# Performance work log

Measured on AMD Instinct MI355X. Metric: run time of the kernel, lower is better.

## Reference

```python
import jax, jax.numpy as jnp
import numpy as np

EMBED_DIM = 512
NUM_TYPES = 26
PER_TYPE = 128
NUM_CODES = NUM_TYPES * PER_TYPE
COMMIT = 0.25
TEMP = 0.07
N_TOKENS = 32768
SAMPLED_PER_TYPE = int(0.1 * PER_TYPE)  # 12


def _normalize(v, axis=-1):
    # matches F.normalize(p=2) with eps clamp
    return v / jnp.clip(jnp.linalg.norm(v, axis=axis, keepdims=True), 1e-12)


def setup_inputs() -> dict:
    key = jax.random.key(0)
    k1, k2, k3, k4 = jax.random.split(key, 4)
    x = jax.random.normal(k1, (N_TOKENS, EMBED_DIM), jnp.float32)
    Q = jax.random.randint(k2, (N_TOKENS,), 0, NUM_TYPES)
    initrange = 1.0 / EMBED_DIM
    emb = jax.random.uniform(k3, (NUM_CODES, EMBED_DIM), jnp.float32, -initrange, initrange)
    emb = _normalize(emb)  # mirrors _initialize_embeddings
    # deterministic stand-in for torch.randperm(num_per_type)[:sampled_num]
    perm = jax.random.permutation(k4, PER_TYPE)[:SAMPLED_PER_TYPE]
    sampled_indices = (jnp.arange(NUM_TYPES)[:, None] * PER_TYPE + perm[None, :]).reshape(-1)
    return {"x": x, "embeddings": emb, "Q": Q, "sampled_indices": sampled_indices}


def _code_indices(xn, embeddings, Q):
    # full [N, num_codes] squared distances, then select the 128-code slab of
    # each token's PTM type and argmin within it (equivalent to the per-type loop)
    d = ((xn ** 2).sum(-1, keepdims=True)
         + (embeddings ** 2).sum(-1)[None, :]
         - 2.0 * (xn @ embeddings.T))                      # [N, NUM_CODES]
    d = d.reshape(xn.shape[0], NUM_TYPES, PER_TYPE)
    d_sel = jnp.take_along_axis(d, Q[:, None, None], axis=1)[:, 0, :]  # [N, PER_TYPE]
    return jnp.argmin(d_sel, axis=1) + Q * PER_TYPE


def _uniform_loss(embeddings, sampled_indices):
    ne = _normalize(embeddings)
    se = ne[sampled_indices]                               # [S, D]
    sim = se @ se.T                                        # [S, S]
    labels = sampled_indices // PER_TYPE
    pos = (labels[None, :] == labels[:, None]).astype(jnp.float32)
    S = sampled_indices.shape[0]
    eye = jnp.eye(S, dtype=bool)
    sim = jnp.where(eye, -jnp.inf, sim)
    sim_exp = jnp.exp(sim / TEMP)                          # exp(-inf) = 0 kills diagonal
    sum_exp = sim_exp.sum(axis=1)
    pos_sum = (sim_exp * pos).sum(axis=1)
    return -jnp.log(pos_sum / sum_exp).mean()


def reference(x, embeddings, Q, sampled_indices):
    xn = _normalize(x)
    idx = _code_indices(xn, embeddings, Q)
    quantized = _normalize(embeddings[idx])
    q_latent = jnp.mean((quantized - jax.lax.stop_gradient(xn)) ** 2)
    e_latent = jnp.mean((xn - jax.lax.stop_gradient(quantized)) ** 2)
    loss = q_latent + COMMIT * e_latent
    uloss = _uniform_loss(embeddings, sampled_indices)
    out = xn + jax.lax.stop_gradient(quantized - xn)       # straight-through
    return out, loss, uloss, idx
```

## Files before the change

### kernel.cpp

```cpp
#include <hip/hip_runtime.h>
#include <math.h>

#define NTOK   32768
#define DIM    512
#define NTYPES 26
#define PT     128
#define NCODES 3328
#define NSAMP  312
#define INV_TEMP (1.0f / 0.07f)
#define MAXTILES 24

typedef __attribute__((ext_vector_type(8))) short short8;
typedef __attribute__((ext_vector_type(4))) float floatx4;

__device__ __forceinline__ void f2bf2(float f, unsigned short& h, unsigned short& l) {
    unsigned u = __float_as_uint(f);
    unsigned hb = (u + 0x7fffu + ((u >> 16) & 1u)) >> 16;
    h = (unsigned short)hb;
    float hf = __uint_as_float(hb << 16);
    float r = f - hf;
    unsigned u2 = __float_as_uint(r);
    l = (unsigned short)((u2 + 0x7fffu + ((u2 >> 16) & 1u)) >> 16);
}

__global__ __launch_bounds__(256) void k_emb(const float* __restrict__ emb,
                                             unsigned short* __restrict__ Bhg,
                                             unsigned short* __restrict__ Blg,
                                             float* __restrict__ sume,
                                             float* __restrict__ rinv,
                                             int* __restrict__ counts,
                                             float* __restrict__ accg) {
    int tid = threadIdx.x;
    if (blockIdx.x == 0) {
        if (tid < NTYPES) counts[tid] = 0;
        if (tid == 32) accg[0] = 0.0f;
        if (tid == 33) accg[1] = 0.0f;
    }
    int wv = tid >> 6, lane = tid & 63;
    int c = blockIdx.x * 4 + wv;
    const float4* row = (const float4*)(emb + (size_t)c * DIM);
    float4 v0 = row[lane * 2], v1 = row[lane * 2 + 1];
    float s = v0.x*v0.x + v0.y*v0.y + v0.z*v0.z + v0.w*v0.w
            + v1.x*v1.x + v1.y*v1.y + v1.z*v1.z + v1.w*v1.w;
    for (int m = 32; m; m >>= 1) s += __shfl_xor(s, m);
    if (lane == 0) {
        sume[c] = s;
        rinv[c] = 1.0f / fmaxf(sqrtf(s), 1e-12f);
    }
    union { short8 v; unsigned short u[8]; } hh, ll;
    f2bf2(v0.x, hh.u[0], ll.u[0]); f2bf2(v0.y, hh.u[1], ll.u[1]);
    f2bf2(v0.z, hh.u[2], ll.u[2]); f2bf2(v0.w, hh.u[3], ll.u[3]);
    f2bf2(v1.x, hh.u[4], ll.u[4]); f2bf2(v1.y, hh.u[5], ll.u[5]);
    f2bf2(v1.z, hh.u[6], ll.u[6]); f2bf2(v1.w, hh.u[7], ll.u[7]);
    *(short8*)(Bhg + (size_t)c * DIM + lane * 8) = hh.v;
    *(short8*)(Blg + (size_t)c * DIM + lane * 8) = ll.v;
}

__global__ __launch_bounds__(256) void k_hist(const int* __restrict__ Q,
                                              int* __restrict__ counts,
                                              int* __restrict__ rank) {
    __shared__ int lbin[NTYPES];
    __shared__ int lbase[NTYPES];
    int tid = threadIdx.x;
    if (tid < NTYPES) lbin[tid] = 0;
    __syncthreads();
    int t = blockIdx.x * 256 + tid;
    int qt = Q[t];
    int lr = atomicAdd(&lbin[qt], 1);
    __syncthreads();
    if (tid < NTYPES) lbase[tid] = atomicAdd(&counts[tid], lbin[tid]);
    __syncthreads();
    rank[t] = lbase[qt] + lr;
}

__global__ __launch_bounds__(256) void k_scatter(const int* __restrict__ Q,
                                                 const int* __restrict__ counts,
                                                 const int* __restrict__ rank,
                                                 int* __restrict__ order,
                                                 int* __restrict__ offsg) {
    __shared__ int offs[NTYPES];
    int tid = threadIdx.x;
    if (tid == 0) {
        int a = 0;
        for (int i = 0; i < NTYPES; i++) {
            offs[i] = a;
            if (blockIdx.x == 0) offsg[i] = a;
            a += counts[i];
        }
        if (blockIdx.x == 0) offsg[NTYPES] = a;
    }
    __syncthreads();
    int t = blockIdx.x * 256 + tid;
    order[offs[Q[t]] + rank[t]] = t;
}

__global__ __launch_bounds__(256, 3) void k_main(const float* __restrict__ x,
                                                 const float* __restrict__ emb,
                                                 const unsigned short* __restrict__ Bhg,
                                                 const unsigned short* __restrict__ Blg,
                                                 const int* __restrict__ order,
                                                 const int* __restrict__ offsg,
                                                 const float* __restrict__ sume,
                                                 const float* __restrict__ rinv,
                                                 float* __restrict__ outbuf,
                                                 float* __restrict__ idxout,
                                                 float* __restrict__ accg) {
    int q = blockIdx.x;
    int tile = blockIdx.y;
    int base = offsg[q];
    int cnt = offsg[q + 1] - base;
    int tstart = tile * 64;
    if (tstart >= cnt) return;
    int nt = min(64, cnt - tstart);

    __shared__ unsigned short Ah[64][72];
    __shared__ unsigned short Al[64][72];
    __shared__ unsigned short Bh[128 * 64];
    __shared__ unsigned short Bl[128 * 64];
    __shared__ int   toks_s[64];
    __shared__ float rn_s[64];
    __shared__ float sume_s[128];
    __shared__ float rinv_s[128];
    __shared__ float redv[64][2];
    __shared__ int   redi[64][2];
    __shared__ int   bestc[64];

    int tid = threadIdx.x;
    int lane = tid & 63;
    int wv = tid >> 6;
    int wm = wv & 1, wn = wv >> 1;
    int lc = lane & 15;
    int q4 = lane >> 4;

    if (tid < 64) toks_s[tid] = order[base + tstart + min(tid, nt - 1)];
    if (tid < 128) {
        sume_s[tid] = sume[q * PT + tid];
        rinv_s[tid] = rinv[q * PT + tid];
    }

    const float* aptr[4];
    int arow = tid >> 4, asg = tid & 15;
#pragma unroll
    for (int i = 0; i < 4; i++) {
        int r = arow + 16 * i;
        int t = order[base + tstart + min(r, nt - 1)];
        aptr[i] = x + (size_t)t * DIM + asg * 4;
    }
    const unsigned short* bh_slab = Bhg + (size_t)q * PT * DIM;
    const unsigned short* bl_slab = Blg + (size_t)q * PT * DIM;
    size_t bofs[4];
#pragma unroll
    for (int i = 0; i < 4; i++) {
        int id = tid + i * 256;
        bofs[i] = (size_t)(id >> 3) * DIM + (id & 7) * 8;
    }

    floatx4 acc[2][4];
#pragma unroll
    for (int mi = 0; mi < 2; mi++)
#pragma unroll
        for (int ni = 0; ni < 4; ni++)
            acc[mi][ni] = (floatx4){0.f, 0.f, 0.f, 0.f};
    float ps[4] = {0.f, 0.f, 0.f, 0.f};

    float4 va[4];
    short8 vbh[4], vbl[4];
#pragma unroll
    for (int i = 0; i < 4; i++) va[i] = *(const float4*)(aptr[i]);
#pragma unroll
    for (int i = 0; i < 4; i++) {
        vbh[i] = *(const short8*)(bh_slab + bofs[i]);
        vbl[i] = *(const short8*)(bl_slab + bofs[i]);
    }

    for (int kc = 0; kc < 8; kc++) {
#pragma unroll
        for (int i = 0; i < 4; i++) {
            int r = arow + 16 * i;
            float4 v = va[i];
            ps[i] = fmaf(v.x, v.x, fmaf(v.y, v.y, fmaf(v.z, v.z, fmaf(v.w, v.w, ps[i]))));
            ushort4 h, l;
            f2bf2(v.x, h.x, l.x); f2bf2(v.y, h.y, l.y);
            f2bf2(v.z, h.z, l.z); f2bf2(v.w, h.w, l.w);
            *(ushort4*)&Ah[r][asg * 4] = h;
            *(ushort4*)&Al[r][asg * 4] = l;
        }
#pragma unroll
        for (int i = 0; i < 4; i++) {
            int id = tid + i * 256;
            int r = id >> 3, p = id & 7;
            int dst = r * 64 + ((p ^ (r & 7)) << 3);
            *(short8*)&Bh[dst] = vbh[i];
            *(short8*)&Bl[dst] = vbl[i];
        }
        __syncthreads();
        if (kc < 7) {
            int k0n = (kc + 1) * 64;
#pragma unroll
            for (int i = 0; i < 4; i++) va[i] = *(const float4*)(aptr[i] + k0n);
#pragma unroll
            for (int i = 0; i < 4; i++) {
                vbh[i] = *(const short8*)(bh_slab + bofs[i] + k0n);
                vbl[i] = *(const short8*)(bl_slab + bofs[i] + k0n);
            }
        }
#pragma unroll
        for (int ks2 = 0; ks2 < 2; ks2++) {
            int ko = ks2 * 32 + q4 * 8;
            int g = ko >> 3;
            short8 ahf[2], alf[2], bhf[4], blf[4];
#pragma unroll
            for (int mi = 0; mi < 2; mi++) {
                int m = wm * 32 + mi * 16 + lc;
                ahf[mi] = *(const short8*)&Ah[m][ko];
                alf[mi] = *(const short8*)&Al[m][ko];
            }
#pragma unroll
            for (int ni = 0; ni < 4; ni++) {
                int n = wn * 64 + ni * 16 + lc;
                int bs = n * 64 + ((g ^ (lc & 7)) << 3);
                bhf[ni] = *(const short8*)&Bh[bs];
                blf[ni] = *(const short8*)&Bl[bs];
            }
#pragma unroll
            for (int mi = 0; mi < 2; mi++)
#pragma unroll
                for (int ni = 0; ni < 4; ni++) {
                    acc[mi][ni] = __builtin_amdgcn_mfma_f32_16x16x32_bf16(ahf[mi], bhf[ni], acc[mi][ni], 0, 0, 0);
                    acc[mi][ni] = __builtin_amdgcn_mfma_f32_16x16x32_bf16(ahf[mi], blf[ni], acc[mi][ni], 0, 0, 0);
                    acc[mi][ni] = __builtin_amdgcn_mfma_f32_16x16x32_bf16(alf[mi], bhf[ni], acc[mi][ni], 0, 0, 0);
                }
        }
        __syncthreads();
    }

#pragma unroll
    for (int m = 1; m <= 8; m <<= 1)
#pragma unroll
        for (int i = 0; i < 4; i++) ps[i] += __shfl_xor(ps[i], m);
    if ((lane & 15) == 0) {
#pragma unroll
        for (int i = 0; i < 4; i++)
            rn_s[arow + 16 * i] = 1.0f / fmaxf(sqrtf(ps[i]), 1e-12f);
    }
    __syncthreads();

#pragma unroll
    for (int mi = 0; mi < 2; mi++) {
#pragma unroll
        for (int r = 0; r < 4; r++) {
            int m = wm * 32 + mi * 16 + q4 * 4 + r;
            float rn2 = -2.0f * rn_s[m];
            float bv = 1e30f; int bc = 0;
#pragma unroll
            for (int ni = 0; ni < 4; ni++) {
                int n = wn * 64 + ni * 16 + lc;
                float d = fmaf(rn2, acc[mi][ni][r], sume_s[n]);
                if (d < bv) { bv = d; bc = n; }
            }
#pragma unroll
            for (int mk = 1; mk <= 8; mk <<= 1) {
                float ov = __shfl_xor(bv, mk);
                int oc = __shfl_xor(bc, mk);
                if (ov < bv || (ov == bv && oc < bc)) { bv = ov; bc = oc; }
            }
            if (lc == 0) { redv[m][wn] = bv; redi[m][wn] = bc; }
        }
    }
    __syncthreads();

    if (tid < 64) {
        float v0 = redv[tid][0], v1 = redv[tid][1];
        int c = (v1 < v0) ? redi[tid][1] : redi[tid][0];
        float bv = fminf(v0, v1);
        bestc[tid] = c;
        float term = 0.0f;
        if (tid < nt) {
            idxout[toks_s[tid]] = (float)(q * PT + c);
            term = 2.0f - (sume_s[c] - bv) * rinv_s[c];
        }
        for (int mk = 32; mk; mk >>= 1) term += __shfl_xor(term, mk);
        if (tid == 0) atomicAdd(&accg[0], term);
    }
    __syncthreads();

    for (int t = wv; t < nt; t += 4) {
        int c = bestc[t];
        int gt = toks_s[t];
        float rv = rinv_s[c];
        const float4* er = (const float4*)(emb + (size_t)(q * PT + c) * DIM);
        float4* orow = (float4*)(outbuf + (size_t)gt * DIM);
#pragma unroll
        for (int s2 = 0; s2 < 2; s2++) {
            float4 ev = er[lane * 2 + s2];
            orow[lane * 2 + s2] = make_float4(ev.x * rv, ev.y * rv, ev.z * rv, ev.w * rv);
        }
    }
}

__global__ __launch_bounds__(256) void k_uloss(const float* __restrict__ emb,
                                               const int* __restrict__ samp,
                                               const float* __restrict__ rinv,
                                               float* __restrict__ accg) {
    __shared__ float rs[4], rp[4];
    int i = blockIdx.x;
    int tid = threadIdx.x;
    int lane = tid & 63, wv = tid >> 6;
    int ci = samp[i];
    float rvi = rinv[ci];
    int labi = ci >> 7;
    const float4* ri = (const float4*)(emb + (size_t)ci * DIM);
    float4 e0 = ri[lane * 2], e1 = ri[lane * 2 + 1];
    float sE = 0.0f, pE = 0.0f;
    for (int j0 = wv; j0 < NSAMP; j0 += 16) {
        float d[4]; int cj[4]; bool val[4];
#pragma unroll
        for (int u = 0; u < 4; u++) {
            int j = j0 + u * 4;
            val[u] = (j < NSAMP) && (j != i);
            int js = val[u] ? j : 0;
            cj[u] = samp[js];
            const float4* rj = (const float4*)(emb + (size_t)cj[u] * DIM);
            float4 f0 = rj[lane * 2], f1 = rj[lane * 2 + 1];
            d[u] = e0.x*f0.x + e0.y*f0.y + e0.z*f0.z + e0.w*f0.w
                 + e1.x*f1.x + e1.y*f1.y + e1.z*f1.z + e1.w*f1.w;
        }
#pragma unroll
        for (int mk = 32; mk; mk >>= 1)
#pragma unroll
            for (int u = 0; u < 4; u++) d[u] += __shfl_xor(d[u], mk);
#pragma unroll
        for (int u = 0; u < 4; u++) {
            float ex = val[u] ? expf(d[u] * rvi * rinv[cj[u]] * INV_TEMP) : 0.0f;
            sE += ex;
            if (val[u] && (cj[u] >> 7) == labi) pE += ex;
        }
    }
    if (lane == 0) { rs[wv] = sE; rp[wv] = pE; }
    __syncthreads();
    if (tid == 0) {
        float S = rs[0] + rs[1] + rs[2] + rs[3];
        float P = rp[0] + rp[1] + rp[2] + rp[3];
        atomicAdd(&accg[1], logf(S) - logf(P));
    }
}

__global__ void k_final(const float* __restrict__ accg, float* __restrict__ lossp) {
    lossp[0] = (1.25f / ((float)NTOK * (float)DIM)) * accg[0];
    lossp[1] = accg[1] / (float)NSAMP;
}

extern "C" void kernel_launch(void* const* d_in, const int* in_sizes, int n_in,
                              void* d_out, int out_size, void* d_ws, size_t ws_size,
                              hipStream_t stream) {
    const float* x   = (const float*)d_in[0];
    const float* emb = (const float*)d_in[1];
    const int* Q     = (const int*)d_in[2];
    const int* samp  = (const int*)d_in[3];

    float* out    = (float*)d_out;
    float* lossp  = out + (size_t)NTOK * DIM;
    float* idxout = out + (size_t)NTOK * DIM + 2;

    unsigned short* Bhg = (unsigned short*)d_ws;
    unsigned short* Blg = Bhg + (size_t)NCODES * DIM;
    float* sume  = (float*)(Blg + (size_t)NCODES * DIM);
    float* rinv  = sume + NCODES;
    int* counts  = (int*)(rinv + NCODES);
    int* offsg   = counts + NTYPES;
    int* rank    = offsg + NTYPES + 1;
    int* order   = rank + NTOK;
    float* accg  = (float*)(order + NTOK);

    k_emb<<<NCODES / 4, 256, 0, stream>>>(emb, Bhg, Blg, sume, rinv, counts, accg);
    k_hist<<<NTOK / 256, 256, 0, stream>>>(Q, counts, rank);
    k_scatter<<<NTOK / 256, 256, 0, stream>>>(Q, counts, rank, order, offsg);
    dim3 gmain(NTYPES, MAXTILES);
    k_main<<<gmain, 256, 0, stream>>>(x, emb, Bhg, Blg, order, offsg, sume, rinv, out, idxout, accg);
    k_uloss<<<NSAMP, 256, 0, stream>>>(emb, samp, rinv, accg);
    k_final<<<1, 1, 0, stream>>>(accg, lossp);
}
```

Baseline: 212.6 us.

## Pre-swizzle codebook into MFMA fragment layout and drop LDS staging in main kernel

The prep kernel now writes the bf16 hi/lo codebook directly in the per-lane MFMA fragment order. Each wave in the main kernel then handles 16 tokens on its own and loads A and B fragments straight from global memory into registers, with no shared-memory tiles or block barriers. Argmin, loss accumulation and output writes are done per wave with shuffles, and launch bounds rise to 4 blocks per CU. This removes LDS traffic and syncs but drops the cross-wave reuse of B, so every wave re-reads the 128-code slab from L2. That raises global/L2 traffic and leaves no software prefetch.

```diff
diff --git a/kernel.cpp b/kernel.cpp
--- a/kernel.cpp
+++ b/kernel.cpp
@@ -52,8 +52,14 @@
     f2bf2(v0.z, hh.u[2], ll.u[2]); f2bf2(v0.w, hh.u[3], ll.u[3]);
     f2bf2(v1.x, hh.u[4], ll.u[4]); f2bf2(v1.y, hh.u[5], ll.u[5]);
     f2bf2(v1.z, hh.u[6], ll.u[6]); f2bf2(v1.w, hh.u[7], ll.u[7]);
-    *(short8*)(Bhg + (size_t)c * DIM + lane * 8) = hh.v;
-    *(short8*)(Blg + (size_t)c * DIM + lane * 8) = ll.v;
+    int qq  = c >> 7;
+    int n   = c & 127;
+    int ni  = n >> 4, lcc = n & 15;
+    int ks2 = lane >> 2, q4d = lane & 3;
+    size_t dst = (size_t)qq * (PT * DIM)
+               + (size_t)(((ks2 * 8 + ni) * 64 + q4d * 16 + lcc) * 8);
+    *(short8*)(Bhg + dst) = hh.v;
+    *(short8*)(Blg + dst) = ll.v;
 }
 
 __global__ __launch_bounds__(256) void k_hist(const int* __restrict__ Q,
@@ -94,7 +100,7 @@
     order[offs[Q[t]] + rank[t]] = t;
 }
 
-__global__ __launch_bounds__(256, 3) void k_main(const float* __restrict__ x,
+__global__ __launch_bounds__(256, 4) void k_main(const float* __restrict__ x,
                                                  const float* __restrict__ emb,
                                                  const unsigned short* __restrict__ Bhg,
                                                  const unsigned short* __restrict__ Blg,
@@ -106,194 +112,112 @@
                                                  float* __restrict__ idxout,
                                                  float* __restrict__ accg) {
     int q = blockIdx.x;
-    int tile = blockIdx.y;
     int base = offsg[q];
     int cnt = offsg[q + 1] - base;
-    int tstart = tile * 64;
+    int wv = threadIdx.x >> 6;
+    int tstart = blockIdx.y * 64 + wv * 16;
     if (tstart >= cnt) return;
-    int nt = min(64, cnt - tstart);
-
-    __shared__ unsigned short Ah[64][72];
-    __shared__ unsigned short Al[64][72];
-    __shared__ unsigned short Bh[128 * 64];
-    __shared__ unsigned short Bl[128 * 64];
-    __shared__ int   toks_s[64];
-    __shared__ float rn_s[64];
-    __shared__ float sume_s[128];
-    __shared__ float rinv_s[128];
-    __shared__ float redv[64][2];
-    __shared__ int   redi[64][2];
-    __shared__ int   bestc[64];
-
-    int tid = threadIdx.x;
-    int lane = tid & 63;
-    int wv = tid >> 6;
-    int wm = wv & 1, wn = wv >> 1;
-    int lc = lane & 15;
-    int q4 = lane >> 4;
-
-    if (tid < 64) toks_s[tid] = order[base + tstart + min(tid, nt - 1)];
-    if (tid < 128) {
-        sume_s[tid] = sume[q * PT + tid];
-        rinv_s[tid] = rinv[q * PT + tid];
-    }
-
-    const float* aptr[4];
-    int arow = tid >> 4, asg = tid & 15;
-#pragma unroll
-    for (int i = 0; i < 4; i++) {
-        int r = arow + 16 * i;
-        int t = order[base + tstart + min(r, nt - 1)];
-        aptr[i] = x + (size_t)t * DIM + asg * 4;
-    }
-    const unsigned short* bh_slab = Bhg + (size_t)q * PT * DIM;
-    const unsigned short* bl_slab = Blg + (size_t)q * PT * DIM;
-    size_t bofs[4];
-#pragma unroll
-    for (int i = 0; i < 4; i++) {
-        int id = tid + i * 256;
-        bofs[i] = (size_t)(id >> 3) * DIM + (id & 7) * 8;
-    }
-
-    floatx4 acc[2][4];
-#pragma unroll
-    for (int mi = 0; mi < 2; mi++)
-#pragma unroll
-        for (int ni = 0; ni < 4; ni++)
-            acc[mi][ni] = (floatx4){0.f, 0.f, 0.f, 0.f};
-    float ps[4] = {0.f, 0.f, 0.f, 0.f};
-
-    float4 va[4];
-    short8 vbh[4], vbl[4];
-#pragma unroll
-    for (int i = 0; i < 4; i++) va[i] = *(const float4*)(aptr[i]);
-#pragma unroll
-    for (int i = 0; i < 4; i++) {
-        vbh[i] = *(const short8*)(bh_slab + bofs[i]);
-        vbl[i] = *(const short8*)(bl_slab + bofs[i]);
-    }
-
-    for (int kc = 0; kc < 8; kc++) {
-#pragma unroll
-        for (int i = 0; i < 4; i++) {
-            int r = arow + 16 * i;
-            float4 v = va[i];
-            ps[i] = fmaf(v.x, v.x, fmaf(v.y, v.y, fmaf(v.z, v.z, fmaf(v.w, v.w, ps[i]))));
-            ushort4 h, l;
-            f2bf2(v.x, h.x, l.x); f2bf2(v.y, h.y, l.y);
-            f2bf2(v.z, h.z, l.z); f2bf2(v.w, h.w, l.w);
-            *(ushort4*)&Ah[r][asg * 4] = h;
-            *(ushort4*)&Al[r][asg * 4] = l;
-        }
-#pragma unroll
-        for (int i = 0; i < 4; i++) {
-            int id = tid + i * 256;
-            int r = id >> 3, p = id & 7;
-            int dst = r * 64 + ((p ^ (r & 7)) << 3);
-            *(short8*)&Bh[dst] = vbh[i];
-            *(short8*)&Bl[dst] = vbl[i];
-        }
-        __syncthreads();
-        if (kc < 7) {
-            int k0n = (kc + 1) * 64;
-#pragma unroll
-            for (int i = 0; i < 4; i++) va[i] = *(const float4*)(aptr[i] + k0n);
-#pragma unroll
-            for (int i = 0; i < 4; i++) {
-                vbh[i] = *(const short8*)(bh_slab + bofs[i] + k0n);
-                vbl[i] = *(const short8*)(bl_slab + bofs[i] + k0n);
+    int ntw = min(16, cnt - tstart);
+
+    int lane = threadIdx.x & 63;
+    int lc = lane & 15, q4 = lane >> 4;
+
+    int tok = order[base + tstart + min(lc, ntw - 1)];
+    const float* ap = x + (size_t)tok * DIM + q4 * 8;
+
+    const unsigned short* bh = Bhg + (size_t)q * (PT * DIM) + lane * 8;
+    const unsigned short* bl = Blg + (size_t)q * (PT * DIM) + lane * 8;
+
+    float sv[8];
+#pragma unroll
+    for (int ni = 0; ni < 8; ni++) sv[ni] = sume[q * PT + ni * 16 + lc];
+
+    floatx4 acc[8];
+#pragma unroll
+    for (int i = 0; i < 8; i++) acc[i] = (floatx4){0.f, 0.f, 0.f, 0.f};
+    float ps = 0.0f;
+
+    for (int ks2 = 0; ks2 < 16; ks2++) {
+        float4 a0 = *(const float4*)(ap);
+        float4 a1 = *(const float4*)(ap + 4);
+        ap += 32;
+        ps = fmaf(a0.x, a0.x, fmaf(a0.y, a0.y, fmaf(a0.z, a0.z, fmaf(a0.w, a0.w, ps))));
+        ps = fmaf(a1.x, a1.x, fmaf(a1.y, a1.y, fmaf(a1.z, a1.z, fmaf(a1.w, a1.w, ps))));
+        union { short8 v; unsigned short u[8]; } ah, al;
+        f2bf2(a0.x, ah.u[0], al.u[0]); f2bf2(a0.y, ah.u[1], al.u[1]);
+        f2bf2(a0.z, ah.u[2], al.u[2]); f2bf2(a0.w, ah.u[3], al.u[3]);
+        f2bf2(a1.x, ah.u[4], al.u[4]); f2bf2(a1.y, ah.u[5], al.u[5]);
+        f2bf2(a1.z, ah.u[6], al.u[6]); f2bf2(a1.w, ah.u[7], al.u[7]);
+
+        const unsigned short* bkh = bh + ks2 * 4096;
+        const unsigned short* bkl = bl + ks2 * 4096;
+#pragma unroll
+        for (int h = 0; h < 2; h++) {
+            short8 bhf[4], blf[4];
+#pragma unroll
+            for (int j = 0; j < 4; j++) {
+                bhf[j] = *(const short8*)(bkh + (h * 4 + j) * 512);
+                blf[j] = *(const short8*)(bkl + (h * 4 + j) * 512);
             }
-        }
-#pragma unroll
-        for (int ks2 = 0; ks2 < 2; ks2++) {
-            int ko = ks2 * 32 + q4 * 8;
-            int g = ko >> 3;
-            short8 ahf[2], alf[2], bhf[4], blf[4];
-#pragma unroll
-            for (int mi = 0; mi < 2; mi++) {
-                int m = wm * 32 + mi * 16 + lc;
-                ahf[mi] = *(const short8*)&Ah[m][ko];
-                alf[mi] = *(const short8*)&Al[m][ko];
+#pragma unroll
+            for (int j = 0; j < 4; j++) {
+                acc[h * 4 + j] = __builtin_amdgcn_mfma_f32_16x16x32_bf16(ah.v, bhf[j], acc[h * 4 + j], 0, 0, 0);
+                acc[h * 4 + j] = __builtin_amdgcn_mfma_f32_16x16x32_bf16(ah.v, blf[j], acc[h * 4 + j], 0, 0, 0);
+                acc[h * 4 + j] = __builtin_amdgcn_mfma_f32_16x16x32_bf16(al.v, bhf[j], acc[h * 4 + j], 0, 0, 0);
             }
-#pragma unroll
-            for (int ni = 0; ni < 4; ni++) {
-                int n = wn * 64 + ni * 16 + lc;
-                int bs = n * 64 + ((g ^ (lc & 7)) << 3);
-                bhf[ni] = *(const short8*)&Bh[bs];
-                blf[ni] = *(const short8*)&Bl[bs];
-            }
-#pragma unroll
-            for (int mi = 0; mi < 2; mi++)
-#pragma unroll
-                for (int ni = 0; ni < 4; ni++) {
-                    acc[mi][ni] = __builtin_amdgcn_mfma_f32_16x16x32_bf16(ahf[mi], bhf[ni], acc[mi][ni], 0, 0, 0);
-                    acc[mi][ni] = __builtin_amdgcn_mfma_f32_16x16x32_bf16(ahf[mi], blf[ni], acc[mi][ni], 0, 0, 0);
-                    acc[mi][ni] = __builtin_amdgcn_mfma_f32_16x16x32_bf16(alf[mi], bhf[ni], acc[mi][ni], 0, 0, 0);
-                }
-        }
-        __syncthreads();
-    }
-
-#pragma unroll
-    for (int m = 1; m <= 8; m <<= 1)
-#pragma unroll
-        for (int i = 0; i < 4; i++) ps[i] += __shfl_xor(ps[i], m);
-    if ((lane & 15) == 0) {
-#pragma unroll
-        for (int i = 0; i < 4; i++)
-            rn_s[arow + 16 * i] = 1.0f / fmaxf(sqrtf(ps[i]), 1e-12f);
-    }
-    __syncthreads();
-
-#pragma unroll
-    for (int mi = 0; mi < 2; mi++) {
+        }
+    }
+
+    ps += __shfl_xor(ps, 16);
+    ps += __shfl_xor(ps, 32);
+    float rnv = 1.0f / fmaxf(sqrtf(ps), 1e-12f);
+
+    float termsum = 0.0f;
+    int bca[4];
+#pragma unroll
+    for (int r = 0; r < 4; r++) {
+        int row = q4 * 4 + r;
+        float rn2 = -2.0f * __shfl(rnv, row);
+        float bv = 1e30f; int bc = 0;
+#pragma unroll
+        for (int ni = 0; ni < 8; ni++) {
+            float d = fmaf(rn2, acc[ni][r], sv[ni]);
+            int n = ni * 16 + lc;
+            if (d < bv) { bv = d; bc = n; }
+        }
+#pragma unroll
+        for (int mk = 1; mk <= 8; mk <<= 1) {
+            float ov = __shfl_xor(bv, mk);
+            int oc = __shfl_xor(bc, mk);
+            if (ov < bv || (ov == bv && oc < bc)) { bv = ov; bc = oc; }
+        }
+        bca[r] = bc;
+        int gt = __shfl(tok, row);
+        if (lc == 0 && row < ntw) {
+            idxout[gt] = (float)(q * PT + bc);
+            float se = sume[q * PT + bc];
+            float rc = rinv[q * PT + bc];
+            termsum += 2.0f - (se - bv) * rc;
+        }
+    }
+    termsum += __shfl_xor(termsum, 16);
+    termsum += __shfl_xor(termsum, 32);
+    if (lane == 0) atomicAdd(&accg[0], termsum);
+
+#pragma unroll
+    for (int g = 0; g < 4; g++) {
 #pragma unroll
         for (int r = 0; r < 4; r++) {
-            int m = wm * 32 + mi * 16 + q4 * 4 + r;
-            float rn2 = -2.0f * rn_s[m];
-            float bv = 1e30f; int bc = 0;
-#pragma unroll
-            for (int ni = 0; ni < 4; ni++) {
-                int n = wn * 64 + ni * 16 + lc;
-                float d = fmaf(rn2, acc[mi][ni][r], sume_s[n]);
-                if (d < bv) { bv = d; bc = n; }
-            }
-#pragma unroll
-            for (int mk = 1; mk <= 8; mk <<= 1) {
-                float ov = __shfl_xor(bv, mk);
-                int oc = __shfl_xor(bc, mk);
-                if (ov < bv || (ov == bv && oc < bc)) { bv = ov; bc = oc; }
-            }
-            if (lc == 0) { redv[m][wn] = bv; redi[m][wn] = bc; }
-        }
-    }
-    __syncthreads();
-
-    if (tid < 64) {
-        float v0 = redv[tid][0], v1 = redv[tid][1];
-        int c = (v1 < v0) ? redi[tid][1] : redi[tid][0];
-        float bv = fminf(v0, v1);
-        bestc[tid] = c;
-        float term = 0.0f;
-        if (tid < nt) {
-            idxout[toks_s[tid]] = (float)(q * PT + c);
-            term = 2.0f - (sume_s[c] - bv) * rinv_s[c];
-        }
-        for (int mk = 32; mk; mk >>= 1) term += __shfl_xor(term, mk);
-        if (tid == 0) atomicAdd(&accg[0], term);
-    }
-    __syncthreads();
-
-    for (int t = wv; t < nt; t += 4) {
-        int c = bestc[t];
-        int gt = toks_s[t];
-        float rv = rinv_s[c];
-        const float4* er = (const float4*)(emb + (size_t)(q * PT + c) * DIM);
-        float4* orow = (float4*)(outbuf + (size_t)gt * DIM);
-#pragma unroll
-        for (int s2 = 0; s2 < 2; s2++) {
-            float4 ev = er[lane * 2 + s2];
-            orow[lane * 2 + s2] = make_float4(ev.x * rv, ev.y * rv, ev.z * rv, ev.w * rv);
+            int row = g * 4 + r;
+            if (row >= ntw) continue;
+            int c = __shfl(bca[r], g * 16);
+            int gt = __shfl(tok, row);
+            float rv = rinv[q * PT + c];
+            const float4* er = (const float4*)(emb + (size_t)(q * PT + c) * DIM);
+            float4* orow = (float4*)(outbuf + (size_t)gt * DIM);
+            float4 e0 = er[lane * 2], e1 = er[lane * 2 + 1];
+            orow[lane * 2]     = make_float4(e0.x * rv, e0.y * rv, e0.z * rv, e0.w * rv);
+            orow[lane * 2 + 1] = make_float4(e1.x * rv, e1.y * rv, e1.z * rv, e1.w * rv);
         }
     }
 }
```

Result: slower. 233.6 us (+9.9%).
